# Kernel tuning notes

Hardware: AMD Instinct MI355X
Metric: run time of the kernel (lower is better)

The kernel has to match this reference:

```python
import jax, jax.numpy as jnp
import numpy as np

N = 50000       # num nodes
E = 800000      # num edges (avg degree 16)
D = 128         # in_dim = hidden_dim = out_dim
C = 10          # n_classes
NOISE_STD = 0.1
LN_EPS = 1e-5


def layer_norm(x, g, b):
    mu = jnp.mean(x, axis=-1, keepdims=True)
    var = jnp.mean((x - mu) ** 2, axis=-1, keepdims=True)
    return (x - mu) * jax.lax.rsqrt(var + LN_EPS) * g + b


def gcn_conv(x, W, b, src, dst, dout_isqrt, din_isqrt):
    # DGL GraphConv, norm='both': h = D_in^{-1/2} A (D_out^{-1/2} x W) + b
    h = (x * dout_isqrt[:, None]) @ W              # [N, D] transform first (in>=out)
    agg = jax.ops.segment_sum(h[src], dst, num_segments=x.shape[0])  # SpMM via gather+scatter
    return agg * din_isqrt[:, None] + b


def setup_inputs() -> dict:
    key = jax.random.key(0)
    ks = jax.random.split(key, 16)
    inv = 1.0 / np.sqrt(D)
    return {
        "feat": jax.random.normal(ks[0], (N, D), jnp.float32),
        "noise": jax.random.normal(ks[1], (N, D), jnp.float32),
        "node_mask": jax.random.bernoulli(ks[2], 0.1, (N,)),
        "src": jax.random.randint(ks[3], (E,), 0, N, jnp.int32),
        "dst": jax.random.randint(ks[4], (E,), 0, N, jnp.int32),
        "mask_token": jax.random.normal(ks[5], (D,), jnp.float32) * inv,
        "W0": jax.random.normal(ks[6], (D, D), jnp.float32) * inv,
        "b0": jnp.zeros((D,), jnp.float32),
        "ln0_g": jnp.ones((D,), jnp.float32),
        "ln0_b": jnp.zeros((D,), jnp.float32),
        "W1": jax.random.normal(ks[7], (D, D), jnp.float32) * inv,
        "b1": jnp.zeros((D,), jnp.float32),
        "ln1_g": jnp.ones((D,), jnp.float32),
        "ln1_b": jnp.zeros((D,), jnp.float32),
        "dec_W1": jax.random.normal(ks[8], (D, D), jnp.float32) * inv,
        "dec_b1": jnp.zeros((D,), jnp.float32),
        "dec_W2": jax.random.normal(ks[9], (D, D), jnp.float32) * inv,
        "dec_b2": jnp.zeros((D,), jnp.float32),
        "cls_W": jax.random.normal(ks[10], (D, C), jnp.float32) * inv,
        "cls_b": jnp.zeros((C,), jnp.float32),
    }


def reference(feat, noise, node_mask, src, dst, mask_token,
              W0, b0, ln0_g, ln0_b, W1, b1, ln1_g, ln1_b,
              dec_W1, dec_b1, dec_W2, dec_b2, cls_W, cls_b):
    n = feat.shape[0]
    ones_e = jnp.ones(src.shape, feat.dtype)
    deg_out = jax.ops.segment_sum(ones_e, src, num_segments=n)
    deg_in = jax.ops.segment_sum(ones_e, dst, num_segments=n)
    dout_isqrt = jnp.where(deg_out > 0, jax.lax.rsqrt(jnp.maximum(deg_out, 1.0)), 0.0)
    din_isqrt = jnp.where(deg_in > 0, jax.lax.rsqrt(jnp.maximum(deg_in, 1.0)), 0.0)

    # node masking + noise injection (eval mode: dropout is identity)
    x_masked = jnp.where(node_mask[:, None], mask_token[None, :], feat) + noise * NOISE_STD

    # encoder: layer 0 (conv -> LN -> ReLU), layer 1 (conv -> LN)
    h = gcn_conv(x_masked, W0, b0, src, dst, dout_isqrt, din_isqrt)
    h = jax.nn.relu(layer_norm(h, ln0_g, ln0_b))
    h = gcn_conv(h, W1, b1, src, dst, dout_isqrt, din_isqrt)
    z = layer_norm(h, ln1_g, ln1_b)

    x_recon = jax.nn.relu(z @ dec_W1 + dec_b1) @ dec_W2 + dec_b2
    logits = z @ cls_W + cls_b
    return (x_recon, feat, node_mask, z, logits)
```

## Files before the change

kernel.cpp:

```cpp
#include <hip/hip_runtime.h>
#include <hip/hip_bf16.h>

#define LN_EPS 1e-5f
#define HB 64
#define HSEG 12800
#define NBLK 128
#define BROWS 64
#define WPSTRIDE 17408

typedef __attribute__((ext_vector_type(8))) short short8;
typedef __attribute__((ext_vector_type(4))) float f32x4;

__device__ __forceinline__ unsigned short f2bf(float f) {
    unsigned int u = __float_as_uint(f);
    u += 0x7fffu + ((u >> 16) & 1u);
    return (unsigned short)(u >> 16);
}
__device__ __forceinline__ unsigned int pack2bf(float a, float b) {
    return (unsigned int)f2bf(a) | ((unsigned int)f2bf(b) << 16);
}
__device__ __forceinline__ float bflo(unsigned int v) { return __uint_as_float(v << 16); }
__device__ __forceinline__ float bfhi(unsigned int v) { return __uint_as_float(v & 0xffff0000u); }

__global__ __launch_bounds__(256) void k_pack(const float* __restrict__ Wa, const float* __restrict__ Wb,
                                              const float* __restrict__ Wc, const float* __restrict__ Wd,
                                              unsigned short* __restrict__ dst) {
    int wsel = blockIdx.x >> 6;
    int idx = (blockIdx.x & 63) * 256 + threadIdx.x;
    const float* W = wsel == 0 ? Wa : wsel == 1 ? Wb : wsel == 2 ? Wc : Wd;
    int c = idx >> 7, kk = idx & 127;
    dst[(size_t)wsel * WPSTRIDE + c * 136 + kk] = f2bf(W[kk * 128 + c]);
}

__global__ __launch_bounds__(512) void k_hist(const int* __restrict__ src, int* __restrict__ partials,
                                              int N, int E) {
    __shared__ int h[HSEG];
    int chunk = blockIdx.x & (HB - 1);
    int seg = blockIdx.x >> 6;
    int lo = seg * HSEG;
    int len = N - lo;
    if (len > HSEG) len = HSEG;
    if (len <= 0) return;
    for (int i = threadIdx.x; i < len; i += 512) h[i] = 0;
    __syncthreads();
    int per = (E + HB - 1) / HB;
    int e0 = chunk * per, e1 = min(e0 + per, E);
    for (int e = e0 + threadIdx.x; e < e1; e += 512) {
        int s = src[e] - lo;
        if ((unsigned)s < (unsigned)len) atomicAdd(&h[s], 1);
    }
    __syncthreads();
    for (int i = threadIdx.x; i < len; i += 512)
        partials[(size_t)chunk * N + lo + i] = h[i];
}

__global__ __launch_bounds__(256) void k_hist_reduce(const int* __restrict__ partials,
                                                     float* __restrict__ doutv, int N) {
    int i = blockIdx.x * 256 + threadIdx.x;
    if (i >= N) return;
    int s = 0;
#pragma unroll
    for (int b = 0; b < HB; ++b) s += partials[(size_t)b * N + i];
    doutv[i] = s > 0 ? 1.0f / sqrtf((float)s) : 0.0f;
}

__global__ __launch_bounds__(256) void k_binA(const int* __restrict__ dst, int* __restrict__ counts,
                                              int nbuck, int E) {
    __shared__ int h[1024];
    for (int i = threadIdx.x; i < nbuck; i += 256) h[i] = 0;
    __syncthreads();
    int per = (E + NBLK - 1) / NBLK;
    int e0 = blockIdx.x * per, e1 = min(e0 + per, E);
    for (int e = e0 + threadIdx.x; e < e1; e += 256) atomicAdd(&h[dst[e] >> 6], 1);
    __syncthreads();
    for (int i = threadIdx.x; i < nbuck; i += 256) counts[(size_t)i * NBLK + blockIdx.x] = h[i];
}

__global__ __launch_bounds__(128) void k_binB1(const int* __restrict__ counts, int* __restrict__ tot) {
    __shared__ int sm[128];
    int t = threadIdx.x;
    sm[t] = counts[(size_t)blockIdx.x * NBLK + t];
    __syncthreads();
#pragma unroll
    for (int o = 64; o >= 1; o >>= 1) {
        if (t < o) sm[t] += sm[t + o];
        __syncthreads();
    }
    if (t == 0) tot[blockIdx.x] = sm[0];
}

__global__ __launch_bounds__(1024) void k_binB2(const int* __restrict__ tot, int* __restrict__ base,
                                                int nbuck, int E) {
    __shared__ int sm[1024];
    int t = threadIdx.x;
    int v = (t < nbuck) ? tot[t] : 0;
    sm[t] = v;
    __syncthreads();
    for (int o = 1; o < 1024; o <<= 1) {
        int u = (t >= o) ? sm[t - o] : 0;
        __syncthreads();
        sm[t] += u;
        __syncthreads();
    }
    if (t < nbuck) base[t] = sm[t] - v;
    if (t == 0) base[nbuck] = E;
}

__global__ __launch_bounds__(128) void k_binB3(const int* __restrict__ counts, const int* __restrict__ base,
                                               int* __restrict__ offs) {
    __shared__ int sm[128];
    int t = threadIdx.x;
    int v = counts[(size_t)blockIdx.x * NBLK + t];
    sm[t] = v;
    __syncthreads();
    for (int o = 1; o < 128; o <<= 1) {
        int u = (t >= o) ? sm[t - o] : 0;
        __syncthreads();
        sm[t] += u;
        __syncthreads();
    }
    offs[(size_t)blockIdx.x * NBLK + t] = base[blockIdx.x] + sm[t] - v;
}

__global__ __launch_bounds__(256) void k_binC(const int* __restrict__ src, const int* __restrict__ dst,
                                              const int* __restrict__ offs, uint2* __restrict__ binned,
                                              int nbuck, int E) {
    __shared__ int cur[1024];
    for (int i = threadIdx.x; i < nbuck; i += 256) cur[i] = offs[(size_t)i * NBLK + blockIdx.x];
    __syncthreads();
    int per = (E + NBLK - 1) / NBLK;
    int e0 = blockIdx.x * per, e1 = min(e0 + per, E);
    for (int e = e0 + threadIdx.x; e < e1; e += 256) {
        int d = dst[e];
        int p = atomicAdd(&cur[d >> 6], 1);
        binned[p] = make_uint2((unsigned)src[e], (unsigned)d);
    }
}

__global__ __launch_bounds__(256) void k_csr(const uint2* __restrict__ binned, const int* __restrict__ base,
                                             int* __restrict__ row_ptr, int* __restrict__ csr_src, int N) {
    __shared__ int hcnt[BROWS], ccur[BROWS];
    int b = blockIdx.x, t = threadIdx.x;
    int e0 = base[b], e1 = base[b + 1];
    if (t < BROWS) hcnt[t] = 0;
    __syncthreads();
    for (int e = e0 + t; e < e1; e += 256)
        atomicAdd(&hcnt[binned[e].y & (BROWS - 1)], 1);
    __syncthreads();
    if (t < BROWS) {
        int acc = 0;
        for (int r = 0; r < t; ++r) acc += hcnt[r];
        ccur[t] = acc;
        int gw = b * BROWS + t;
        if (gw <= N) row_ptr[gw] = e0 + acc;
    }
    __syncthreads();
    for (int e = e0 + t; e < e1; e += 256) {
        uint2 ed = binned[e];
        int p = atomicAdd(&ccur[ed.y & (BROWS - 1)], 1);
        csr_src[e0 + p] = (int)ed.x;
    }
}

__global__ __launch_bounds__(256) void k_prep(const float* __restrict__ feat, const float* __restrict__ noise,
                                              const int* __restrict__ mask, const float* __restrict__ token,
                                              unsigned short* __restrict__ xs, float* __restrict__ feat_out,
                                              float* __restrict__ mask_out, int n) {
    int i = blockIdx.x * blockDim.x + threadIdx.x;
    int total = n * 32;
    if (i >= total) return;
    int row = i >> 5, q = i & 31;
    float4 f = ((const float4*)feat)[i];
    float4 nz = ((const float4*)noise)[i];
    bool m = mask[row] != 0;
    float4 b = f;
    if (m) b = ((const float4*)token)[q];
    uint2 p;
    p.x = pack2bf(b.x + 0.1f * nz.x, b.y + 0.1f * nz.y);
    p.y = pack2bf(b.z + 0.1f * nz.z, b.w + 0.1f * nz.w);
    ((uint2*)xs)[i] = p;
    ((float4*)feat_out)[i] = f;
    if (q == 0) mask_out[row] = m ? 1.0f : 0.0f;
}

template <int EPI, int OUT_BF16, int DOUT>
__global__ __launch_bounds__(256) void k_gemm_mfma(const unsigned short* __restrict__ A,
                                                   const unsigned short* __restrict__ Wp,
                                                   const float* __restrict__ bias,
                                                   const float* __restrict__ dscale,
                                                   void* __restrict__ Cout, int n) {
    __shared__ uint4 BtV[2176];
    unsigned short* Bt = (unsigned short*)BtV;
    int tid = threadIdx.x;
    const uint4* Wv = (const uint4*)Wp;
    for (int i = tid; i < 2176; i += 256) BtV[i] = Wv[i];
    __syncthreads();

    int wid = tid >> 6, lane = tid & 63;
    int q = lane >> 4, m = lane & 15;
    int r0 = blockIdx.x * 128 + wid * 32;

    f32x4 acc[2][8];
#pragma unroll
    for (int i = 0; i < 2; ++i)
#pragma unroll
        for (int j = 0; j < 8; ++j) acc[i][j] = (f32x4){0.f, 0.f, 0.f, 0.f};

#pragma unroll
    for (int ks = 0; ks < 4; ++ks) {
        int k0 = ks * 32 + q * 8;
        short8 a[2];
#pragma unroll
        for (int i = 0; i < 2; ++i) {
            int row = r0 + i * 16 + m;
            if (row > n - 1) row = n - 1;
            a[i] = *(const short8*)(A + (size_t)row * 128 + k0);
        }
        short8 b[8];
#pragma unroll
        for (int j = 0; j < 8; ++j)
            b[j] = *(const short8*)(&Bt[(j * 16 + m) * 136 + k0]);
#pragma unroll
        for (int i = 0; i < 2; ++i)
#pragma unroll
            for (int j = 0; j < 8; ++j)
                acc[i][j] = __builtin_amdgcn_mfma_f32_16x16x32_bf16(a[i], b[j], acc[i][j], 0, 0, 0);
    }

    float bv[8];
    if (EPI >= 1) {
#pragma unroll
        for (int j = 0; j < 8; ++j) bv[j] = bias[j * 16 + m];
    }

#pragma unroll
    for (int i = 0; i < 2; ++i) {
#pragma unroll
        for (int r = 0; r < 4; ++r) {
            int row = r0 + i * 16 + q * 4 + r;
            if (row < n) {
                float ds = DOUT ? dscale[row] : 1.0f;
#pragma unroll
                for (int j = 0; j < 8; ++j) {
                    float v = acc[i][j][r];
                    if (DOUT) v *= ds;
                    if (EPI >= 1) v += bv[j];
                    if (EPI == 2) v = fmaxf(v, 0.0f);
                    if (OUT_BF16)
                        ((unsigned short*)Cout)[(size_t)row * 128 + j * 16 + m] = f2bf(v);
                    else
                        ((float*)Cout)[(size_t)row * 128 + j * 16 + m] = v;
                }
            }
        }
    }
}

template <int MODE>
__global__ __launch_bounds__(256) void k_agg_ln(const unsigned short* __restrict__ H,
                                                const int* __restrict__ row_ptr,
                                                const int* __restrict__ csr_src,
                                                const float* __restrict__ cb, const float* __restrict__ g,
                                                const float* __restrict__ bt,
                                                float* __restrict__ out_f32, unsigned short* __restrict__ out_bf,
                                                int n) {
    int gw = (blockIdx.x * blockDim.x + threadIdx.x) >> 6;
    int lane = threadIdx.x & 63;
    if (gw >= n) return;
    int beg = row_ptr[gw], end = row_ptr[gw + 1];
    int cnt = end - beg;
    const unsigned int* Hu = (const unsigned int*)H;
    float ax0 = 0.f, ay0 = 0.f, ax1 = 0.f, ay1 = 0.f;
    float ax2 = 0.f, ay2 = 0.f, ax3 = 0.f, ay3 = 0.f;
    for (int c0 = beg; c0 < end; c0 += 64) {
        int m = end - c0;
        if (m > 64) m = 64;
        int myidx = (lane < m) ? csr_src[c0 + lane] : 0;
        int k = 0;
        for (; k + 7 < m; k += 8) {
            int s0 = __shfl(myidx, k + 0), s1 = __shfl(myidx, k + 1);
            int s2 = __shfl(myidx, k + 2), s3 = __shfl(myidx, k + 3);
            int s4 = __shfl(myidx, k + 4), s5 = __shfl(myidx, k + 5);
            int s6 = __shfl(myidx, k + 6), s7 = __shfl(myidx, k + 7);
            unsigned int v0 = Hu[(size_t)s0 * 64 + lane];
            unsigned int v1 = Hu[(size_t)s1 * 64 + lane];
            unsigned int v2 = Hu[(size_t)s2 * 64 + lane];
            unsigned int v3 = Hu[(size_t)s3 * 64 + lane];
            unsigned int v4 = Hu[(size_t)s4 * 64 + lane];
            unsigned int v5 = Hu[(size_t)s5 * 64 + lane];
            unsigned int v6 = Hu[(size_t)s6 * 64 + lane];
            unsigned int v7 = Hu[(size_t)s7 * 64 + lane];
            ax0 += bflo(v0); ay0 += bfhi(v0);
            ax1 += bflo(v1); ay1 += bfhi(v1);
            ax2 += bflo(v2); ay2 += bfhi(v2);
            ax3 += bflo(v3); ay3 += bfhi(v3);
            ax0 += bflo(v4); ay0 += bfhi(v4);
            ax1 += bflo(v5); ay1 += bfhi(v5);
            ax2 += bflo(v6); ay2 += bfhi(v6);
            ax3 += bflo(v7); ay3 += bfhi(v7);
        }
        for (; k < m; ++k) {
            int s0 = __shfl(myidx, k);
            unsigned int v0 = Hu[(size_t)s0 * 64 + lane];
            ax0 += bflo(v0); ay0 += bfhi(v0);
        }
    }
    int d0 = lane * 2;
    float sc = cnt > 0 ? 1.0f / sqrtf((float)cnt) : 0.0f;
    float2 cbv = *(const float2*)(cb + d0);
    float2 x;
    x.x = (ax0 + ax1 + ax2 + ax3) * sc + cbv.x;
    x.y = (ay0 + ay1 + ay2 + ay3) * sc + cbv.y;

    float s = x.x + x.y;
#pragma unroll
    for (int mm = 32; mm >= 1; mm >>= 1) s += __shfl_xor(s, mm, 64);
    float mu = s * (1.0f / 128.0f);
    float dx = x.x - mu, dy = x.y - mu;
    float v = dx * dx + dy * dy;
#pragma unroll
    for (int mm = 32; mm >= 1; mm >>= 1) v += __shfl_xor(v, mm, 64);
    float inv = 1.0f / sqrtf(v * (1.0f / 128.0f) + LN_EPS);
    float2 gv = *(const float2*)(g + d0);
    float2 bv = *(const float2*)(bt + d0);
    float y0 = dx * inv * gv.x + bv.x;
    float y1 = dy * inv * gv.y + bv.y;
    if (MODE == 1) {
        y0 = fmaxf(y0, 0.0f);
        y1 = fmaxf(y1, 0.0f);
    } else {
        *(float2*)(out_f32 + (size_t)gw * 128 + d0) = make_float2(y0, y1);
    }
    ((unsigned int*)out_bf)[(size_t)gw * 64 + lane] = pack2bf(y0, y1);
}

__global__ __launch_bounds__(256) void k_cls(const unsigned short* __restrict__ Z, const float* __restrict__ W,
                                             const float* __restrict__ b, float* __restrict__ out,
                                             int n, int C) {
    int gpos = blockIdx.x * blockDim.x + threadIdx.x;
    int row = gpos >> 4, c = gpos & 15;
    if (row >= n || c >= C) return;
    const unsigned int* zr = (const unsigned int*)(Z + (size_t)row * 128);
    float acc = b[c];
#pragma unroll 8
    for (int kk = 0; kk < 64; ++kk) {
        unsigned int v = zr[kk];
        acc = fmaf(bflo(v), W[(2 * kk) * C + c], acc);
        acc = fmaf(bfhi(v), W[(2 * kk + 1) * C + c], acc);
    }
    out[(size_t)row * C + c] = acc;
}

extern "C" void kernel_launch(void* const* d_in, const int* in_sizes, int n_in,
                              void* d_out, int out_size, void* d_ws, size_t ws_size,
                              hipStream_t stream) {
    const float* feat  = (const float*)d_in[0];
    const float* noise = (const float*)d_in[1];
    const int*   nmask = (const int*)d_in[2];
    const int*   src   = (const int*)d_in[3];
    const int*   dst   = (const int*)d_in[4];
    const float* token = (const float*)d_in[5];
    const float* W0    = (const float*)d_in[6];
    const float* b0    = (const float*)d_in[7];
    const float* ln0g  = (const float*)d_in[8];
    const float* ln0b  = (const float*)d_in[9];
    const float* W1    = (const float*)d_in[10];
    const float* b1    = (const float*)d_in[11];
    const float* ln1g  = (const float*)d_in[12];
    const float* ln1b  = (const float*)d_in[13];
    const float* dW1   = (const float*)d_in[14];
    const float* db1   = (const float*)d_in[15];
    const float* dW2   = (const float*)d_in[16];
    const float* db2   = (const float*)d_in[17];
    const float* cW    = (const float*)d_in[18];
    const float* cbias = (const float*)d_in[19];

    const int N = in_sizes[0] / 128;
    const int E = in_sizes[3];
    const int C = in_sizes[19];
    const size_t ND = (size_t)N * 128;
    const int NBUCK = (N + BROWS - 1) / BROWS;
    const int NSEG = (N + HSEG - 1) / HSEG;

    float* out       = (float*)d_out;
    float* out_recon = out;
    float* out_feat  = out + ND;
    float* out_mask  = out + 2 * ND;
    float* out_z     = out + 2 * ND + N;
    float* out_log   = out + 3 * ND + N;

    char* w = (char*)d_ws;
    unsigned short* bufX = (unsigned short*)w; w += ND * 2;
    unsigned short* bufH = (unsigned short*)w; w += ND * 2;
    unsigned short* zbf  = (unsigned short*)w; w += ND * 2;
    unsigned short* wpack = (unsigned short*)w; w += (size_t)4 * WPSTRIDE * 2;
    float* doutv   = (float*)w; w += (size_t)N * 4;
    int* row_ptr   = (int*)w;   w += (size_t)(N + 4) * 4;
    int* csr_src   = (int*)w;   w += (size_t)E * 4;
    int* scratch   = (int*)w;

    int* partials = scratch;
    uint2* binned = (uint2*)scratch;
    int* counts = scratch + (size_t)2 * E;
    int* tot    = counts + (size_t)NBUCK * NBLK;
    int* base   = tot + NBUCK;
    int* offs   = base + NBUCK + 2;

    int nb = (N + 255) / 256;

    k_pack<<<256, 256, 0, stream>>>(W0, W1, dW1, dW2, wpack);

    k_hist<<<HB * NSEG, 512, 0, stream>>>(src, partials, N, E);
    k_hist_reduce<<<nb, 256, 0, stream>>>(partials, doutv, N);

    k_binA<<<NBLK, 256, 0, stream>>>(dst, counts, NBUCK, E);
    k_binB1<<<NBUCK, 128, 0, stream>>>(counts, tot);
    k_binB2<<<1, 1024, 0, stream>>>(tot, base, NBUCK, E);
    k_binB3<<<NBUCK, 128, 0, stream>>>(counts, base, offs);
    k_binC<<<NBLK, 256, 0, stream>>>(src, dst, offs, binned, NBUCK, E);
    k_csr<<<NBUCK, 256, 0, stream>>>(binned, base, row_ptr, csr_src, N);

    k_prep<<<(N * 32 + 255) / 256, 256, 0, stream>>>(feat, noise, nmask, token,
                                                     bufX, out_feat, out_mask, N);

    int gb = (N + 127) / 128;
    int rb = (N * 64 + 255) / 256;

    k_gemm_mfma<0, 1, 1><<<gb, 256, 0, stream>>>(bufX, wpack + 0 * WPSTRIDE, nullptr, doutv, bufH, N);
    k_agg_ln<1><<<rb, 256, 0, stream>>>(bufH, row_ptr, csr_src, b0, ln0g, ln0b, nullptr, bufX, N);

    k_gemm_mfma<0, 1, 1><<<gb, 256, 0, stream>>>(bufX, wpack + 1 * WPSTRIDE, nullptr, doutv, bufH, N);
    k_agg_ln<0><<<rb, 256, 0, stream>>>(bufH, row_ptr, csr_src, b1, ln1g, ln1b, out_z, zbf, N);

    k_gemm_mfma<2, 1, 0><<<gb, 256, 0, stream>>>(zbf, wpack + 2 * WPSTRIDE, db1, nullptr, bufX, N);
    k_gemm_mfma<1, 0, 0><<<gb, 256, 0, stream>>>(bufX, wpack + 3 * WPSTRIDE, db2, nullptr, out_recon, N);

    k_cls<<<(N * 16 + 255) / 256, 256, 0, stream>>>(zbf, cW, cbias, out_log, N, C);
}
```

Measured before the change: 218.0 us.

## Merge preprocessing and classifier launches into fewer multi-role kernels

Folds weight packing, dst bucket counting and input prep into one launch that dispatches on block index. Merges the degree reduce and the bucket-total scans into a single launch using wave shuffles. Runs the classifier head as extra blocks inside the first decoder GEMM launch. The aim is to cut launch count and inter-kernel gaps, but the counts buffer is moved past the partials region so the two no longer alias.

```diff
diff --git a/kernel.cpp b/kernel.cpp
--- a/kernel.cpp
+++ b/kernel.cpp
@@ -21,16 +21,6 @@
 }
 __device__ __forceinline__ float bflo(unsigned int v) { return __uint_as_float(v << 16); }
 __device__ __forceinline__ float bfhi(unsigned int v) { return __uint_as_float(v & 0xffff0000u); }
-
-__global__ __launch_bounds__(256) void k_pack(const float* __restrict__ Wa, const float* __restrict__ Wb,
-                                              const float* __restrict__ Wc, const float* __restrict__ Wd,
-                                              unsigned short* __restrict__ dst) {
-    int wsel = blockIdx.x >> 6;
-    int idx = (blockIdx.x & 63) * 256 + threadIdx.x;
-    const float* W = wsel == 0 ? Wa : wsel == 1 ? Wb : wsel == 2 ? Wc : Wd;
-    int c = idx >> 7, kk = idx & 127;
-    dst[(size_t)wsel * WPSTRIDE + c * 136 + kk] = f2bf(W[kk * 128 + c]);
-}
 
 __global__ __launch_bounds__(512) void k_hist(const int* __restrict__ src, int* __restrict__ partials,
                                               int N, int E) {
@@ -54,119 +44,40 @@
         partials[(size_t)chunk * N + lo + i] = h[i];
 }
 
-__global__ __launch_bounds__(256) void k_hist_reduce(const int* __restrict__ partials,
-                                                     float* __restrict__ doutv, int N) {
-    int i = blockIdx.x * 256 + threadIdx.x;
-    if (i >= N) return;
-    int s = 0;
-#pragma unroll
-    for (int b = 0; b < HB; ++b) s += partials[(size_t)b * N + i];
-    doutv[i] = s > 0 ? 1.0f / sqrtf((float)s) : 0.0f;
-}
-
-__global__ __launch_bounds__(256) void k_binA(const int* __restrict__ dst, int* __restrict__ counts,
-                                              int nbuck, int E) {
+__global__ __launch_bounds__(256) void k_front(const int* __restrict__ dst, int* __restrict__ counts,
+                                               const float* __restrict__ Wa, const float* __restrict__ Wb,
+                                               const float* __restrict__ Wc, const float* __restrict__ Wd,
+                                               unsigned short* __restrict__ wpack,
+                                               const float* __restrict__ feat, const float* __restrict__ noise,
+                                               const int* __restrict__ mask, const float* __restrict__ token,
+                                               unsigned short* __restrict__ xs, float* __restrict__ feat_out,
+                                               float* __restrict__ mask_out,
+                                               int nbuck, int E, int n) {
     __shared__ int h[1024];
-    for (int i = threadIdx.x; i < nbuck; i += 256) h[i] = 0;
-    __syncthreads();
-    int per = (E + NBLK - 1) / NBLK;
-    int e0 = blockIdx.x * per, e1 = min(e0 + per, E);
-    for (int e = e0 + threadIdx.x; e < e1; e += 256) atomicAdd(&h[dst[e] >> 6], 1);
-    __syncthreads();
-    for (int i = threadIdx.x; i < nbuck; i += 256) counts[(size_t)i * NBLK + blockIdx.x] = h[i];
-}
-
-__global__ __launch_bounds__(128) void k_binB1(const int* __restrict__ counts, int* __restrict__ tot) {
-    __shared__ int sm[128];
-    int t = threadIdx.x;
-    sm[t] = counts[(size_t)blockIdx.x * NBLK + t];
-    __syncthreads();
-#pragma unroll
-    for (int o = 64; o >= 1; o >>= 1) {
-        if (t < o) sm[t] += sm[t + o];
+    int bid = blockIdx.x;
+    int tid = threadIdx.x;
+    if (bid < NBLK) {
+        for (int i = tid; i < nbuck; i += 256) h[i] = 0;
         __syncthreads();
-    }
-    if (t == 0) tot[blockIdx.x] = sm[0];
-}
-
-__global__ __launch_bounds__(1024) void k_binB2(const int* __restrict__ tot, int* __restrict__ base,
-                                                int nbuck, int E) {
-    __shared__ int sm[1024];
-    int t = threadIdx.x;
-    int v = (t < nbuck) ? tot[t] : 0;
-    sm[t] = v;
-    __syncthreads();
-    for (int o = 1; o < 1024; o <<= 1) {
-        int u = (t >= o) ? sm[t - o] : 0;
+        int per = (E + NBLK - 1) / NBLK;
+        int e0 = bid * per, e1 = min(e0 + per, E);
+        for (int e = e0 + tid; e < e1; e += 256) atomicAdd(&h[dst[e] >> 6], 1);
         __syncthreads();
-        sm[t] += u;
-        __syncthreads();
-    }
-    if (t < nbuck) base[t] = sm[t] - v;
-    if (t == 0) base[nbuck] = E;
-}
-
-__global__ __launch_bounds__(128) void k_binB3(const int* __restrict__ counts, const int* __restrict__ base,
-                                               int* __restrict__ offs) {
-    __shared__ int sm[128];
-    int t = threadIdx.x;
-    int v = counts[(size_t)blockIdx.x * NBLK + t];
-    sm[t] = v;
-    __syncthreads();
-    for (int o = 1; o < 128; o <<= 1) {
-        int u = (t >= o) ? sm[t - o] : 0;
-        __syncthreads();
-        sm[t] += u;
-        __syncthreads();
-    }
-    offs[(size_t)blockIdx.x * NBLK + t] = base[blockIdx.x] + sm[t] - v;
-}
-
-__global__ __launch_bounds__(256) void k_binC(const int* __restrict__ src, const int* __restrict__ dst,
-                                              const int* __restrict__ offs, uint2* __restrict__ binned,
-                                              int nbuck, int E) {
-    __shared__ int cur[1024];
-    for (int i = threadIdx.x; i < nbuck; i += 256) cur[i] = offs[(size_t)i * NBLK + blockIdx.x];
-    __syncthreads();
-    int per = (E + NBLK - 1) / NBLK;
-    int e0 = blockIdx.x * per, e1 = min(e0 + per, E);
-    for (int e = e0 + threadIdx.x; e < e1; e += 256) {
-        int d = dst[e];
-        int p = atomicAdd(&cur[d >> 6], 1);
-        binned[p] = make_uint2((unsigned)src[e], (unsigned)d);
-    }
-}
-
-__global__ __launch_bounds__(256) void k_csr(const uint2* __restrict__ binned, const int* __restrict__ base,
-                                             int* __restrict__ row_ptr, int* __restrict__ csr_src, int N) {
-    __shared__ int hcnt[BROWS], ccur[BROWS];
-    int b = blockIdx.x, t = threadIdx.x;
-    int e0 = base[b], e1 = base[b + 1];
-    if (t < BROWS) hcnt[t] = 0;
-    __syncthreads();
-    for (int e = e0 + t; e < e1; e += 256)
-        atomicAdd(&hcnt[binned[e].y & (BROWS - 1)], 1);
-    __syncthreads();
-    if (t < BROWS) {
-        int acc = 0;
-        for (int r = 0; r < t; ++r) acc += hcnt[r];
-        ccur[t] = acc;
-        int gw = b * BROWS + t;
-        if (gw <= N) row_ptr[gw] = e0 + acc;
-    }
-    __syncthreads();
-    for (int e = e0 + t; e < e1; e += 256) {
-        uint2 ed = binned[e];
-        int p = atomicAdd(&ccur[ed.y & (BROWS - 1)], 1);
-        csr_src[e0 + p] = (int)ed.x;
-    }
-}
-
-__global__ __launch_bounds__(256) void k_prep(const float* __restrict__ feat, const float* __restrict__ noise,
-                                              const int* __restrict__ mask, const float* __restrict__ token,
-                                              unsigned short* __restrict__ xs, float* __restrict__ feat_out,
-                                              float* __restrict__ mask_out, int n) {
-    int i = blockIdx.x * blockDim.x + threadIdx.x;
+        for (int i = tid; i < nbuck; i += 256) counts[(size_t)i * NBLK + bid] = h[i];
+        return;
+    }
+    bid -= NBLK;
+    if (bid < 256) {
+        int idx = bid * 256 + tid;
+        int wsel = idx >> 14;
+        int within = idx & 16383;
+        const float* W = wsel == 0 ? Wa : wsel == 1 ? Wb : wsel == 2 ? Wc : Wd;
+        int c = within >> 7, kk = within & 127;
+        wpack[(size_t)wsel * WPSTRIDE + c * 136 + kk] = f2bf(W[kk * 128 + c]);
+        return;
+    }
+    bid -= 256;
+    int i = bid * 256 + tid;
     int total = n * 32;
     if (i >= total) return;
     int row = i >> 5, q = i & 31;
@@ -183,6 +94,101 @@
     if (q == 0) mask_out[row] = m ? 1.0f : 0.0f;
 }
 
+__global__ __launch_bounds__(1024) void k_mid(const int* __restrict__ partials, float* __restrict__ doutv,
+                                              const int* __restrict__ counts, int* __restrict__ base,
+                                              int* __restrict__ offs, int N, int nbuck, int E, int nr) {
+    int t = threadIdx.x;
+    if ((int)blockIdx.x < nr) {
+        int i = blockIdx.x * 1024 + t;
+        if (i >= N) return;
+        int s = 0;
+#pragma unroll
+        for (int b = 0; b < HB; ++b) s += partials[(size_t)b * N + i];
+        doutv[i] = s > 0 ? 1.0f / sqrtf((float)s) : 0.0f;
+        return;
+    }
+    __shared__ int sm[1024];
+    __shared__ int bs[1024];
+    int wv = t >> 6, ln = t & 63;
+    sm[t] = 0;
+    __syncthreads();
+    for (int b = wv; b < nbuck; b += 16) {
+        int v0 = counts[(size_t)b * NBLK + ln];
+        int v1 = counts[(size_t)b * NBLK + 64 + ln];
+        int s = v0 + v1;
+#pragma unroll
+        for (int o = 32; o >= 1; o >>= 1) s += __shfl_xor(s, o, 64);
+        if (ln == 0) sm[b] = s;
+    }
+    __syncthreads();
+    int v = sm[t];
+    for (int o = 1; o < 1024; o <<= 1) {
+        int u = (t >= o) ? sm[t - o] : 0;
+        __syncthreads();
+        sm[t] += u;
+        __syncthreads();
+    }
+    int excl = sm[t] - v;
+    bs[t] = excl;
+    if (t < nbuck) base[t] = excl;
+    if (t == 0) base[nbuck] = E;
+    __syncthreads();
+    for (int b = wv; b < nbuck; b += 16) {
+        int v0 = counts[(size_t)b * NBLK + ln];
+        int v1 = counts[(size_t)b * NBLK + 64 + ln];
+        int s0 = v0;
+#pragma unroll
+        for (int o = 1; o < 64; o <<= 1) { int u = __shfl_up(s0, o, 64); if (ln >= o) s0 += u; }
+        int tot0 = __shfl(s0, 63, 64);
+        int s1 = v1;
+#pragma unroll
+        for (int o = 1; o < 64; o <<= 1) { int u = __shfl_up(s1, o, 64); if (ln >= o) s1 += u; }
+        int bb = bs[b];
+        offs[(size_t)b * NBLK + ln] = bb + (s0 - v0);
+        offs[(size_t)b * NBLK + 64 + ln] = bb + tot0 + (s1 - v1);
+    }
+}
+
+__global__ __launch_bounds__(256) void k_binC(const int* __restrict__ src, const int* __restrict__ dst,
+                                              const int* __restrict__ offs, uint2* __restrict__ binned,
+                                              int nbuck, int E) {
+    __shared__ int cur[1024];
+    for (int i = threadIdx.x; i < nbuck; i += 256) cur[i] = offs[(size_t)i * NBLK + blockIdx.x];
+    __syncthreads();
+    int per = (E + NBLK - 1) / NBLK;
+    int e0 = blockIdx.x * per, e1 = min(e0 + per, E);
+    for (int e = e0 + threadIdx.x; e < e1; e += 256) {
+        int d = dst[e];
+        int p = atomicAdd(&cur[d >> 6], 1);
+        binned[p] = make_uint2((unsigned)src[e], (unsigned)d);
+    }
+}
+
+__global__ __launch_bounds__(256) void k_csr(const uint2* __restrict__ binned, const int* __restrict__ base,
+                                             int* __restrict__ row_ptr, int* __restrict__ csr_src, int N) {
+    __shared__ int hcnt[BROWS], ccur[BROWS];
+    int b = blockIdx.x, t = threadIdx.x;
+    int e0 = base[b], e1 = base[b + 1];
+    if (t < BROWS) hcnt[t] = 0;
+    __syncthreads();
+    for (int e = e0 + t; e < e1; e += 256)
+        atomicAdd(&hcnt[binned[e].y & (BROWS - 1)], 1);
+    __syncthreads();
+    if (t < BROWS) {
+        int acc = 0;
+        for (int r = 0; r < t; ++r) acc += hcnt[r];
+        ccur[t] = acc;
+        int gw = b * BROWS + t;
+        if (gw <= N) row_ptr[gw] = e0 + acc;
+    }
+    __syncthreads();
+    for (int e = e0 + t; e < e1; e += 256) {
+        uint2 ed = binned[e];
+        int p = atomicAdd(&ccur[ed.y & (BROWS - 1)], 1);
+        csr_src[e0 + p] = (int)ed.x;
+    }
+}
+
 template <int EPI, int OUT_BF16, int DOUT>
 __global__ __launch_bounds__(256) void k_gemm_mfma(const unsigned short* __restrict__ A,
                                                    const unsigned short* __restrict__ Wp,
@@ -250,6 +256,87 @@
                         ((unsigned short*)Cout)[(size_t)row * 128 + j * 16 + m] = f2bf(v);
                     else
                         ((float*)Cout)[(size_t)row * 128 + j * 16 + m] = v;
+                }
+            }
+        }
+    }
+}
+
+__global__ __launch_bounds__(256) void k_gemm_cls(const unsigned short* __restrict__ A,
+                                                  const unsigned short* __restrict__ Wp,
+                                                  const float* __restrict__ bias,
+                                                  void* __restrict__ Cout,
+                                                  const float* __restrict__ cW, const float* __restrict__ cbias,
+                                                  float* __restrict__ logits,
+                                                  int n, int C, int gb) {
+    __shared__ uint4 BtV[2176];
+    unsigned short* Bt = (unsigned short*)BtV;
+    int tid = threadIdx.x;
+    if ((int)blockIdx.x >= gb) {
+        int gpos = ((int)blockIdx.x - gb) * 256 + tid;
+        int row = gpos >> 4, c = gpos & 15;
+        if (row >= n || c >= C) return;
+        const unsigned int* zr = (const unsigned int*)(A + (size_t)row * 128);
+        float acc = cbias[c];
+#pragma unroll 8
+        for (int kk = 0; kk < 64; ++kk) {
+            unsigned int v = zr[kk];
+            acc = fmaf(bflo(v), cW[(2 * kk) * C + c], acc);
+            acc = fmaf(bfhi(v), cW[(2 * kk + 1) * C + c], acc);
+        }
+        logits[(size_t)row * C + c] = acc;
+        return;
+    }
+    const uint4* Wv = (const uint4*)Wp;
+    for (int i = tid; i < 2176; i += 256) BtV[i] = Wv[i];
+    __syncthreads();
+
+    int wid = tid >> 6, lane = tid & 63;
+    int q = lane >> 4, m = lane & 15;
+    int r0 = blockIdx.x * 128 + wid * 32;
+
+    f32x4 acc[2][8];
+#pragma unroll
+    for (int i = 0; i < 2; ++i)
+#pragma unroll
+        for (int j = 0; j < 8; ++j) acc[i][j] = (f32x4){0.f, 0.f, 0.f, 0.f};
+
+#pragma unroll
+    for (int ks = 0; ks < 4; ++ks) {
+        int k0 = ks * 32 + q * 8;
+        short8 a[2];
+#pragma unroll
+        for (int i = 0; i < 2; ++i) {
+            int row = r0 + i * 16 + m;
+            if (row > n - 1) row = n - 1;
+            a[i] = *(const short8*)(A + (size_t)row * 128 + k0);
+        }
+        short8 b[8];
+#pragma unroll
+        for (int j = 0; j < 8; ++j)
+            b[j] = *(const short8*)(&Bt[(j * 16 + m) * 136 + k0]);
+#pragma unroll
+        for (int i = 0; i < 2; ++i)
+#pragma unroll
+            for (int j = 0; j < 8; ++j)
+                acc[i][j] = __builtin_amdgcn_mfma_f32_16x16x32_bf16(a[i], b[j], acc[i][j], 0, 0, 0);
+    }
+
+    float bv[8];
+#pragma unroll
+    for (int j = 0; j < 8; ++j) bv[j] = bias[j * 16 + m];
+
+#pragma unroll
+    for (int i = 0; i < 2; ++i) {
+#pragma unroll
+        for (int r = 0; r < 4; ++r) {
+            int row = r0 + i * 16 + q * 4 + r;
+            if (row < n) {
+#pragma unroll
+                for (int j = 0; j < 8; ++j) {
+                    float v = acc[i][j][r] + bv[j];
+                    v = fmaxf(v, 0.0f);
+                    ((unsigned short*)Cout)[(size_t)row * 128 + j * 16 + m] = f2bf(v);
                 }
             }
         }
@@ -334,23 +421,6 @@
     ((unsigned int*)out_bf)[(size_t)gw * 64 + lane] = pack2bf(y0, y1);
 }
 
-__global__ __launch_bounds__(256) void k_cls(const unsigned short* __restrict__ Z, const float* __restrict__ W,
-                                             const float* __restrict__ b, float* __restrict__ out,
-                                             int n, int C) {
-    int gpos = blockIdx.x * blockDim.x + threadIdx.x;
-    int row = gpos >> 4, c = gpos & 15;
-    if (row >= n || c >= C) return;
-    const unsigned int* zr = (const unsigned int*)(Z + (size_t)row * 128);
-    float acc = b[c];
-#pragma unroll 8
-    for (int kk = 0; kk < 64; ++kk) {
-        unsigned int v = zr[kk];
-        acc = fmaf(bflo(v), W[(2 * kk) * C + c], acc);
-        acc = fmaf(bfhi(v), W[(2 * kk + 1) * C + c], acc);
-    }
-    out[(size_t)row * C + c] = acc;
-}
-
 extern "C" void kernel_launch(void* const* d_in, const int* in_sizes, int n_in,
                               void* d_out, int out_size, void* d_ws, size_t ws_size,
                               hipStream_t stream) {
@@ -402,27 +472,24 @@
     int* partials = scratch;
     uint2* binned = (uint2*)scratch;
     int* counts = scratch + (size_t)2 * E;
+    counts = scratch + (size_t)HB * N;
     int* tot    = counts + (size_t)NBUCK * NBLK;
     int* base   = tot + NBUCK;
     int* offs   = base + NBUCK + 2;
 
-    int nb = (N + 255) / 256;
-
-    k_pack<<<256, 256, 0, stream>>>(W0, W1, dW1, dW2, wpack);
-
     k_hist<<<HB * NSEG, 512, 0, stream>>>(src, partials, N, E);
-    k_hist_reduce<<<nb, 256, 0, stream>>>(partials, doutv, N);
-
-    k_binA<<<NBLK, 256, 0, stream>>>(dst, counts, NBUCK, E);
-    k_binB1<<<NBUCK, 128, 0, stream>>>(counts, tot);
-    k_binB2<<<1, 1024, 0, stream>>>(tot, base, NBUCK, E);
-    k_binB3<<<NBUCK, 128, 0, stream>>>(counts, base, offs);
+
+    int prep_blocks = (N * 32 + 255) / 256;
+    k_front<<<NBLK + 256 + prep_blocks, 256, 0, stream>>>(dst, counts, W0, W1, dW1, dW2, wpack,
+                                                          feat, noise, nmask, token,
+                                                          bufX, out_feat, out_mask, NBUCK, E, N);
+
+    int nr = (N + 1023) / 1024;
+    k_mid<<<nr + 1, 1024, 0, stream>>>(partials, doutv, counts, base, offs, N, NBUCK, E, nr);
+
     k_binC<<<NBLK, 256, 0, stream>>>(src, dst, offs, binned, NBUCK, E);
     k_csr<<<NBUCK, 256, 0, stream>>>(binned, base, row_ptr, csr_src, N);
 
-    k_prep<<<(N * 32 + 255) / 256, 256, 0, stream>>>(feat, noise, nmask, token,
-                                                     bufX, out_feat, out_mask, N);
-
     int gb = (N + 127) / 128;
     int rb = (N * 64 + 255) / 256;
 
@@ -432,8 +499,9 @@
     k_gemm_mfma<0, 1, 1><<<gb, 256, 0, stream>>>(bufX, wpack + 1 * WPSTRIDE, nullptr, doutv, bufH, N);
     k_agg_ln<0><<<rb, 256, 0, stream>>>(bufH, row_ptr, csr_src, b1, ln1g, ln1b, out_z, zbf, N);
 
-    k_gemm_mfma<2, 1, 0><<<gb, 256, 0, stream>>>(zbf, wpack + 2 * WPSTRIDE, db1, nullptr, bufX, N);
+    int cls_blocks = (N * 16 + 255) / 256;
+    k_gemm_cls<<<gb + cls_blocks, 256, 0, stream>>>(zbf, wpack + 2 * WPSTRIDE, db1, bufX,
+                                                    cW, cbias, out_log, N, C, gb);
+
     k_gemm_mfma<1, 0, 0><<<gb, 256, 0, stream>>>(bufX, wpack + 3 * WPSTRIDE, db2, nullptr, out_recon, N);
-
-    k_cls<<<(N * 16 + 255) / 256, 256, 0, stream>>>(zbf, cW, cbias, out_log, N, C);
-}
+}
```

After: 257.9 us. +18.3%, slower.
